# Kernel optimization log

Measured on AMD Instinct MI355X. Metric: run time of the kernel, lower is better.

## Reference

```python
import jax, jax.numpy as jnp
import numpy as np

N_NODES = 50000
N_EDGES = 1600000
IN_CH = 128
HID = 32
HEADS = 3
OUT_CH = 32
NEG_SLOPE = 0.2


def setup_inputs() -> dict:
    key = jax.random.key(0)
    ks = jax.random.split(key, 12)
    s = 0.05
    x = jax.random.normal(ks[0], (N_NODES, IN_CH), dtype=jnp.float32)
    edge_index = jax.random.randint(ks[1], (2, N_EDGES), 0, N_NODES, dtype=jnp.int64)
    W1 = jax.random.normal(ks[2], (IN_CH, HEADS * HID), dtype=jnp.float32) * s
    att_src1 = jax.random.normal(ks[3], (HEADS, HID), dtype=jnp.float32) * s
    att_dst1 = jax.random.normal(ks[4], (HEADS, HID), dtype=jnp.float32) * s
    b1 = jnp.zeros((HEADS * HID,), dtype=jnp.float32)
    W2 = jax.random.normal(ks[5], (HEADS * HID, OUT_CH), dtype=jnp.float32) * s
    att_src2 = jax.random.normal(ks[6], (1, OUT_CH), dtype=jnp.float32) * s
    att_dst2 = jax.random.normal(ks[7], (1, OUT_CH), dtype=jnp.float32) * s
    b2 = jnp.zeros((OUT_CH,), dtype=jnp.float32)
    Wp = jax.random.normal(ks[8], (OUT_CH, 1), dtype=jnp.float32) * s
    bp = jnp.zeros((1,), dtype=jnp.float32)
    return dict(x=x, edge_index=edge_index, W1=W1, att_src1=att_src1,
                att_dst1=att_dst1, b1=b1, W2=W2, att_src2=att_src2,
                att_dst2=att_dst2, b2=b2, Wp=Wp, bp=bp)


def gat_layer(x, src, dst, W, a_src, a_dst, b, heads, out_ch, concat):
    # PyG GATConv semantics: per-head linear, edge attention with leaky_relu,
    # softmax over incoming edges per destination node, scatter-add aggregate.
    N = x.shape[0]
    h = (x @ W).reshape(N, heads, out_ch)                 # [N,H,C]
    a_s = jnp.einsum('nhc,hc->nh', h, a_src)              # [N,H]
    a_d = jnp.einsum('nhc,hc->nh', h, a_dst)              # [N,H]
    e = jax.nn.leaky_relu(a_s[src] + a_d[dst], NEG_SLOPE) # [E,H]
    m = jax.ops.segment_max(e, dst, num_segments=N)       # stable softmax per dst
    p = jnp.exp(e - m[dst])
    s = jax.ops.segment_sum(p, dst, num_segments=N)
    alpha = p / (s[dst] + 1e-16)                          # [E,H]
    msg = h[src] * alpha[:, :, None]                      # [E,H,C]
    out = jax.ops.segment_sum(msg, dst, num_segments=N)   # [N,H,C]
    out = out.reshape(N, heads * out_ch) if concat else out.mean(axis=1)
    return out + b


def reference(x, edge_index, W1, att_src1, att_dst1, b1, W2, att_src2,
              att_dst2, b2, Wp, bp):
    N = x.shape[0]
    loop = jnp.arange(N, dtype=edge_index.dtype)
    src = jnp.concatenate([edge_index[0], loop])  # add self-loops (PyG default)
    dst = jnp.concatenate([edge_index[1], loop])
    h = gat_layer(x, src, dst, W1, att_src1, att_dst1, b1, HEADS, HID, True)
    h = jax.nn.elu(h)
    h = gat_layer(h, src, dst, W2, att_src2, att_dst2, b2, 1, OUT_CH, False)
    prob = jax.nn.sigmoid(h @ Wp + bp)                    # [N,1]
    return prob
```

## Files before the change

kernel.cpp:

```cpp
#include <hip/hip_runtime.h>
#include <hip/hip_bf16.h>
#include <math.h>


#define IN_CH 128
#define HID 32
#define HEADS 3
#define OUT_CH 32
#define NEG_SLOPE 0.2f

#define NBUCK_SHIFT 6
#define NBUCK_NODES 64
#define BCAP 2560
#define EPB 4096

typedef unsigned int uint;
typedef unsigned short ushort;
typedef short v8s __attribute__((ext_vector_type(8)));
typedef float v4f __attribute__((ext_vector_type(4)));
typedef uint v3u __attribute__((ext_vector_type(3)));

static __device__ __forceinline__ uint f2bf(float f) {
    uint u = __float_as_uint(f);
    return (u + 0x7FFFu + ((u >> 16) & 1u)) >> 16;
}
static __device__ __forceinline__ uint pk4fp8(float a, float b, float c, float d) {
    int r = 0;
    r = __builtin_amdgcn_cvt_pk_fp8_f32(a, b, r, false);
    r = __builtin_amdgcn_cvt_pk_fp8_f32(c, d, r, true);
    return (uint)r;
}
static __device__ __forceinline__ float elu_f(float o) {
    return o > 0.f ? o : __expf(o) - 1.f;
}
static __device__ __forceinline__ float frcp(float x) {
    return __builtin_amdgcn_rcpf(x);
}

#define LDA 136
#define LDC 100


__global__ __launch_bounds__(256) void k_pre(const float* __restrict__ W1,
                                             ushort* __restrict__ w1t,
                                             int* __restrict__ gcur) {
    int b = blockIdx.x, t = threadIdx.x;
    if (b < 12) {
        int base = b * 1024 + t * 4;
        #pragma unroll
        for (int j = 0; j < 4; ++j) {
            int idx = base + j;
            int n = idx >> 7, k = idx & 127;
            w1t[idx] = (ushort)f2bf(W1[k * 96 + n]);
        }
    } else {
        int i = (b - 12) * 256 + t;
        if (i < 1024) gcur[i] = 0;
    }
}


__global__ __launch_bounds__(256) void k_g1b(const float* __restrict__ x,
                                             const ushort* __restrict__ w1t,
                                             const float* __restrict__ as,
                                             const float* __restrict__ ad,
                                             uint* __restrict__ h1u,
                                             float* __restrict__ a_d1p,
                                             const int* __restrict__ ei,
                                             int E, int Etot, int B2, int G1,
                                             int* __restrict__ gcur,
                                             uint* __restrict__ stage, int N) {
    __shared__ __attribute__((aligned(16))) char raw[64 * LDC * 4];
    int tid = threadIdx.x;

    if ((int)blockIdx.x >= G1) {
        int* hist     = (int*)raw;
        int* runStart = hist + 1024;
        int* rankCtr  = runStart + 1024;
        for (int i = tid; i < 1024; i += 256) { hist[i] = 0; rankCtr[i] = 0; }
        __syncthreads();
        int base = ((int)blockIdx.x - G1) * EPB;

        uint rec[16];
        #pragma unroll
        for (int i = 0; i < 16; ++i) {
            int e = base + tid + i * 256;
            uint r = 0xFFFFFFFFu;
            if (e < Etot) {
                int s, d;
                if (e < E) { s = ei[e]; d = ei[E + e]; }
                else       { s = e - E; d = s; }
                r = ((uint)d << 16) | (uint)s;
                atomicAdd(&hist[d >> NBUCK_SHIFT], 1);
            }
            rec[i] = r;
        }
        __syncthreads();
        for (int i = tid; i < B2; i += 256) {
            int c = hist[i];
            if (c) runStart[i] = atomicAdd(&gcur[i], c);
        }
        __syncthreads();
        #pragma unroll
        for (int i = 0; i < 16; ++i) {
            uint r = rec[i];
            if (r != 0xFFFFFFFFu) {
                int b = (int)(r >> 16) >> NBUCK_SHIFT;
                int pos = runStart[b] + atomicAdd(&rankCtr[b], 1);
                if (pos < BCAP)
                    stage[(size_t)b * BCAP + pos] = r & 0x003FFFFFu;
            }
        }
        return;
    }

    ushort* sA  = (ushort*)raw;
    float*  sC  = (float*)raw;
    int b0 = blockIdx.x * 64;

    uint* sA32 = (uint*)sA;
    #pragma unroll
    for (int i = 0; i < 8; ++i) {
        int g = tid + i * 256;
        int row = g >> 5, c4 = g & 31;
        float4 v = make_float4(0.f, 0.f, 0.f, 0.f);
        int gn = b0 + row;
        if (gn < N) v = *(const float4*)(x + (size_t)gn * IN_CH + c4 * 4);
        sA32[row * 68 + c4 * 2]     = f2bf(v.x) | (f2bf(v.y) << 16);
        sA32[row * 68 + c4 * 2 + 1] = f2bf(v.z) | (f2bf(v.w) << 16);
    }
    __syncthreads();

    int l = tid & 63, w = tid >> 6;
    int m15 = l & 15, q = l >> 4;

    v8s afr[4];
    const ushort* arow = sA + (w * 16 + m15) * LDA + q * 8;
    #pragma unroll
    for (int kc = 0; kc < 4; ++kc) afr[kc] = *(const v8s*)(arow + kc * 32);

    v4f acc[6];
    #pragma unroll
    for (int cg = 0; cg < 6; ++cg) {
        acc[cg] = (v4f){0.f, 0.f, 0.f, 0.f};
        const ushort* browg = w1t + (cg * 16 + m15) * 128 + q * 8;
        #pragma unroll
        for (int kc = 0; kc < 4; ++kc) {
            v8s bfr = *(const v8s*)(browg + kc * 32);
            acc[cg] = __builtin_amdgcn_mfma_f32_16x16x32_bf16(afr[kc], bfr, acc[cg], 0, 0, 0);
        }
    }
    __syncthreads();
    #pragma unroll
    for (int cg = 0; cg < 6; ++cg) {
        int col = cg * 16 + m15;
        #pragma unroll
        for (int r = 0; r < 4; ++r)
            sC[(w * 16 + q * 4 + r) * LDC + col] = acc[cg][r];
    }
    __syncthreads();

    if (tid < 192) {
        int ln = tid / 3, h = tid - ln * 3;
        int node = b0 + ln;
        if (node < N) {
            const float* vs = as + h * 32;
            const float* vd = ad + h * 32;
            const float* row = sC + ln * LDC + h * 32;
            float4 s4 = make_float4(0.f, 0.f, 0.f, 0.f);
            float4 d4 = make_float4(0.f, 0.f, 0.f, 0.f);
            #pragma unroll
            for (int c = 0; c < 8; ++c) {
                float4 r = *(const float4*)(row + 4 * c);
                float4 a = *(const float4*)(vs + 4 * c);
                float4 bb = *(const float4*)(vd + 4 * c);
                s4.x += r.x * a.x;  s4.y += r.y * a.y;
                s4.z += r.z * a.z;  s4.w += r.w * a.w;
                d4.x += r.x * bb.x; d4.y += r.y * bb.y;
                d4.z += r.z * bb.z; d4.w += r.w * bb.w;
            }
            float s = (s4.x + s4.y) + (s4.z + s4.w);
            float d = (d4.x + d4.y) + (d4.z + d4.w);
            ((float*)h1u)[(size_t)node * 32 + 24 + h] = s;
            a_d1p[node * 4 + h] = d;
        }
    }
    {
        int node = tid >> 2, part = tid & 3;
        int gn = b0 + node;
        if (gn < N) {
            const float* row = sC + node * LDC;
            uint tmp[6];
            #pragma unroll
            for (int jj = 0; jj < 6; ++jj) {
                int j = part * 6 + jj;
                int dd = j / 3, slot = j - dd * 3;
                const float* p = row + slot * 32 + dd * 4;
                tmp[jj] = pk4fp8(p[0], p[1], p[2], p[3]);
            }
            uint* dst = h1u + (size_t)gn * 32 + part * 6;
            *(uint2*)(dst + 0) = make_uint2(tmp[0], tmp[1]);
            *(uint2*)(dst + 2) = make_uint2(tmp[2], tmp[3]);
            *(uint2*)(dst + 4) = make_uint2(tmp[4], tmp[5]);
        }
    }
}


__global__ __launch_bounds__(256) void k_sort(const uint* __restrict__ stage,
                                              const int* __restrict__ gcur,
                                              int* __restrict__ offs,
                                              ushort* __restrict__ edges,
                                              int N, int Etot, int B2) {
    __shared__ uint items[BCAP];
    __shared__ int red[256];
    __shared__ int lofs[NBUCK_NODES + 1];
    __shared__ int cursors[NBUCK_NODES];
    int t = threadIdx.x;
    int b = blockIdx.x;

    int partial = 0;
    for (int i = t; i < b; i += 256) partial += gcur[i];
    red[t] = partial;
    if (t < NBUCK_NODES) cursors[t] = 0;
    __syncthreads();
    #pragma unroll
    for (int s = 128; s > 0; s >>= 1) {
        if (t < s) red[t] += red[t + s];
        __syncthreads();
    }
    int gbase = red[0];
    int cnt = gcur[b]; if (cnt > BCAP) cnt = BCAP;

    for (int i = t; i < cnt; i += 256) items[i] = stage[(size_t)b * BCAP + i];
    __syncthreads();
    for (int i = t; i < cnt; i += 256) atomicAdd(&cursors[items[i] >> 16], 1);
    __syncthreads();
    if (t == 0) {
        int run = 0;
        for (int i = 0; i < NBUCK_NODES; ++i) { int v = cursors[i]; lofs[i] = run; run += v; }
        lofs[NBUCK_NODES] = run;
    }
    __syncthreads();
    int nodeBase = b << NBUCK_SHIFT;
    if (t < NBUCK_NODES && nodeBase + t < N) offs[nodeBase + t] = gbase + lofs[t];
    if (b == B2 - 1 && t == 0) offs[N] = Etot;
    if (t < NBUCK_NODES) cursors[t] = 0;
    __syncthreads();
    for (int i = t; i < cnt; i += 256) {
        uint it = items[i];
        int ln = (int)(it >> 16);
        int r = atomicAdd(&cursors[ln], 1);
        edges[gbase + lofs[ln] + r] = (ushort)(it & 0xFFFFu);
    }
}


#define W2LD 36

__global__ __launch_bounds__(256) void k_agg1g2(const int* __restrict__ offs,
                                                const ushort* __restrict__ edges,
                                                const uint* __restrict__ h1u,
                                                const float* __restrict__ a_d1p,
                                                const float* __restrict__ b1,
                                                const float* __restrict__ W2,
                                                const float* __restrict__ as2,
                                                const float* __restrict__ ad2,
                                                uint* __restrict__ h2u,
                                                float* __restrict__ a_d2, int N) {
    __shared__ __attribute__((aligned(16))) float sW2[96 * W2LD];
    __shared__ float ss2[32], sd2[32];
    __shared__ float rowbuf[8][96];

    int tid = threadIdx.x;
    #pragma unroll
    for (int i = 0; i < 3; ++i) {
        int gg = tid + i * 256;
        int k = gg >> 3, c4i = gg & 7;
        *(float4*)&sW2[k * W2LD + c4i * 4] = *(const float4*)(W2 + k * 32 + c4i * 4);
    }
    if (tid < 32) { ss2[tid] = as2[tid]; sd2[tid] = ad2[tid]; }
    __syncthreads();

    int w = tid >> 6;
    int lane = tid & 63;
    int half = lane >> 5, hl = lane & 31;
    int node = blockIdx.x * 8 + w * 2 + half;
    bool nvalid = node < N;
    int nodeC = nvalid ? node : (N - 1);
    int g = hl >> 3, d = hl & 7;
    const float4 adv = *(const float4*)(a_d1p + nodeC * 4);

    int off0 = offs[nodeC], off1 = offs[nodeC + 1];
    int deg = off1 - off0;
    if (deg < 0) deg = 0;
    int nIt = (deg + 3) >> 2;
    int nItO = __shfl_xor(nIt, 32);
    int itMax = nIt > nItO ? nIt : nItO;

    float a00 = 0.f, a01 = 0.f, a02 = 0.f, a03 = 0.f;
    float a10 = 0.f, a11 = 0.f, a12 = 0.f, a13 = 0.f;
    float a20 = 0.f, a21 = 0.f, a22 = 0.f, a23 = 0.f;
    float d0 = 0.f, d1 = 0.f, d2 = 0.f;

    #pragma unroll 2
    for (int i = 0; i < itMax; ++i) {
        int e = i * 4 + g;
        bool act = e < deg;
        int eidx = off0 + (act ? e : 0);
        uint src = (uint)edges[eidx];
        const uint* hr = h1u + src * 32u;
        float4 af = *(const float4*)(hr + 24);
        v3u wv = *(const v3u*)(hr + 3 * d);
        float z0 = af.x + adv.x, z1 = af.y + adv.y, z2 = af.z + adv.z;
        z0 = fmaxf(z0, NEG_SLOPE * z0);
        z1 = fmaxf(z1, NEG_SLOPE * z1);
        z2 = fmaxf(z2, NEG_SLOPE * z2);
        float p0 = __expf(z0), p1 = __expf(z1), p2 = __expf(z2);
        p0 = act ? p0 : 0.f;
        p1 = act ? p1 : 0.f;
        p2 = act ? p2 : 0.f;
        { auto lo = __builtin_amdgcn_cvt_pk_f32_fp8((int)wv[0], false);
          auto hi = __builtin_amdgcn_cvt_pk_f32_fp8((int)wv[0], true);
          a00 += p0 * lo[0]; a01 += p0 * lo[1];
          a02 += p0 * hi[0]; a03 += p0 * hi[1]; }
        { auto lo = __builtin_amdgcn_cvt_pk_f32_fp8((int)wv[1], false);
          auto hi = __builtin_amdgcn_cvt_pk_f32_fp8((int)wv[1], true);
          a10 += p1 * lo[0]; a11 += p1 * lo[1];
          a12 += p1 * hi[0]; a13 += p1 * hi[1]; }
        { auto lo = __builtin_amdgcn_cvt_pk_f32_fp8((int)wv[2], false);
          auto hi = __builtin_amdgcn_cvt_pk_f32_fp8((int)wv[2], true);
          a20 += p2 * lo[0]; a21 += p2 * lo[1];
          a22 += p2 * hi[0]; a23 += p2 * hi[1]; }
        d0 += p0; d1 += p1; d2 += p2;
    }

    #define REDF(v) { v += __shfl_xor(v, 8); v += __shfl_xor(v, 16); }
    REDF(a00) REDF(a01) REDF(a02) REDF(a03)
    REDF(a10) REDF(a11) REDF(a12) REDF(a13)
    REDF(a20) REDF(a21) REDF(a22) REDF(a23)
    REDF(d0) REDF(d1) REDF(d2)
    #undef REDF

    int rbrow = w * 2 + half;
    if (hl < 8) {
        float r0 = frcp(d0 + 1e-16f);
        float r1 = frcp(d1 + 1e-16f);
        float r2 = frcp(d2 + 1e-16f);
        float4 bv0 = *(const float4*)(b1 + 4 * hl);
        float4 bv1 = *(const float4*)(b1 + 32 + 4 * hl);
        float4 bv2 = *(const float4*)(b1 + 64 + 4 * hl);
        float4 v;
        v.x = elu_f(a00 * r0 + bv0.x);
        v.y = elu_f(a01 * r0 + bv0.y);
        v.z = elu_f(a02 * r0 + bv0.z);
        v.w = elu_f(a03 * r0 + bv0.w);
        *(float4*)&rowbuf[rbrow][4 * hl] = v;
        v.x = elu_f(a10 * r1 + bv1.x);
        v.y = elu_f(a11 * r1 + bv1.y);
        v.z = elu_f(a12 * r1 + bv1.z);
        v.w = elu_f(a13 * r1 + bv1.w);
        *(float4*)&rowbuf[rbrow][32 + 4 * hl] = v;
        v.x = elu_f(a20 * r2 + bv2.x);
        v.y = elu_f(a21 * r2 + bv2.y);
        v.z = elu_f(a22 * r2 + bv2.z);
        v.w = elu_f(a23 * r2 + bv2.w);
        *(float4*)&rowbuf[rbrow][64 + 4 * hl] = v;
    }

    int c4 = hl & 7, kg = hl >> 3;
    float4 accv = make_float4(0.f, 0.f, 0.f, 0.f);
    const float* rb = &rowbuf[rbrow][kg * 24];
    const float* wb = &sW2[kg * 24 * W2LD + c4 * 4];
    #pragma unroll 24
    for (int i = 0; i < 24; ++i) {
        float rv = rb[i];
        float4 wvv = *(const float4*)(wb + i * W2LD);
        accv.x += rv * wvv.x; accv.y += rv * wvv.y;
        accv.z += rv * wvv.z; accv.w += rv * wvv.w;
    }
    #define REDF(c) { c += __shfl_xor(c, 8); c += __shfl_xor(c, 16); }
    REDF(accv.x) REDF(accv.y) REDF(accv.z) REDF(accv.w)
    #undef REDF

    float4 sv = *(const float4*)&ss2[c4 * 4];
    float4 dv = *(const float4*)&sd2[c4 * 4];
    float ps = accv.x * sv.x + accv.y * sv.y + accv.z * sv.z + accv.w * sv.w;
    float pd = accv.x * dv.x + accv.y * dv.y + accv.z * dv.z + accv.w * dv.w;
    ps += __shfl_xor(ps, 1); ps += __shfl_xor(ps, 2); ps += __shfl_xor(ps, 4);
    pd += __shfl_xor(pd, 1); pd += __shfl_xor(pd, 2); pd += __shfl_xor(pd, 4);
    if (nvalid && hl < 8) {
        h2u[(size_t)node * 16 + c4] = pk4fp8(accv.x, accv.y, accv.z, accv.w);
        if (hl == 0) {
            ((float*)h2u)[(size_t)node * 16 + 8] = ps;
            a_d2[node] = pd;
        }
    }
}


__global__ __launch_bounds__(256) void k_agg2f(const int* __restrict__ offs,
                                               const ushort* __restrict__ edges,
                                               const uint* __restrict__ h2u,
                                               const float* __restrict__ a_d2,
                                               const float* __restrict__ b2,
                                               const float* __restrict__ Wp,
                                               const float* __restrict__ bp,
                                               float* __restrict__ out, int N) {
    int tid = threadIdx.x;
    int w = tid >> 6;
    int lane = tid & 63;
    int half = lane >> 5, hl = lane & 31;
    int node = blockIdx.x * 8 + w * 2 + half;
    bool nvalid = node < N;
    int nodeC = nvalid ? node : (N - 1);
    int g = hl >> 3, d = hl & 7;
    const float ad2u = a_d2[nodeC];

    int off0 = offs[nodeC], off1 = offs[nodeC + 1];
    int deg = off1 - off0;
    if (deg < 0) deg = 0;
    int nIt = (deg + 3) >> 2;
    int nItO = __shfl_xor(nIt, 32);
    int itMax = nIt > nItO ? nIt : nItO;

    float c0 = 0.f, c1 = 0.f, c2 = 0.f, c3 = 0.f, den = 0.f;

    #pragma unroll 2
    for (int i = 0; i < itMax; ++i) {
        int e = i * 4 + g;
        bool act = e < deg;
        int eidx = off0 + (act ? e : 0);
        uint src = (uint)edges[eidx];
        const uint* hr = h2u + src * 16u;
        float zf = *(const float*)(hr + 8);
        uint wvv = hr[d];
        float z = zf + ad2u;
        z = fmaxf(z, NEG_SLOPE * z);
        float p = __expf(z);
        p = act ? p : 0.f;
        auto lo = __builtin_amdgcn_cvt_pk_f32_fp8((int)wvv, false);
        auto hi = __builtin_amdgcn_cvt_pk_f32_fp8((int)wvv, true);
        c0 += p * lo[0]; c1 += p * lo[1];
        c2 += p * hi[0]; c3 += p * hi[1];
        den += p;
    }

    #define REDF(v) { v += __shfl_xor(v, 8); v += __shfl_xor(v, 16); }
    REDF(c0) REDF(c1) REDF(c2) REDF(c3) REDF(den)
    #undef REDF

    float4 bv = *(const float4*)(b2 + 4 * d);
    float4 wv = *(const float4*)(Wp + 4 * d);
    float r = frcp(den + 1e-16f);
    float v = (c0 * r + bv.x) * wv.x + (c1 * r + bv.y) * wv.y +
              (c2 * r + bv.z) * wv.z + (c3 * r + bv.w) * wv.w;
    v += __shfl_xor(v, 1);
    v += __shfl_xor(v, 2);
    v += __shfl_xor(v, 4);
    if (nvalid && hl == 0)
        out[node] = frcp(1.f + __expf(-(v + bp[0])));
}


extern "C" void kernel_launch(void* const* d_in, const int* in_sizes, int n_in,
                              void* d_out, int out_size, void* d_ws, size_t ws_size,
                              hipStream_t stream) {
    const float* x      = (const float*)d_in[0];
    const int*   ei     = (const int*)d_in[1];
    const float* W1     = (const float*)d_in[2];
    const float* att_s1 = (const float*)d_in[3];
    const float* att_d1 = (const float*)d_in[4];
    const float* b1     = (const float*)d_in[5];
    const float* W2     = (const float*)d_in[6];
    const float* att_s2 = (const float*)d_in[7];
    const float* att_d2 = (const float*)d_in[8];
    const float* b2     = (const float*)d_in[9];
    const float* Wp     = (const float*)d_in[10];
    const float* bp     = (const float*)d_in[11];
    float* out = (float*)d_out;

    const int N = in_sizes[0] / IN_CH;
    const int E = in_sizes[1] / 2;
    const int Etot = E + N;
    const int B2 = (N + NBUCK_NODES - 1) >> NBUCK_SHIFT;
    const int G1 = (N + 63) / 64;
    const int BK = (Etot + EPB - 1) / EPB;

    float*  ws    = (float*)d_ws;
    uint*   h1u   = (uint*)ws;
    float*  a_d1p = ws + (size_t)N * 32;
    int*    offs  = (int*)(a_d1p + (size_t)N * 4);
    ushort* edges = (ushort*)(offs + (N + 1));
    int*    gcur  = (int*)(edges + (((size_t)Etot + 1) & ~(size_t)1));
    uint*   stage = (uint*)(gcur + 1024);
    uint*   h2u   = stage + (size_t)B2 * BCAP;
    float*  a_d2  = (float*)(h2u + (size_t)N * 16);
    ushort* w1t   = (ushort*)(a_d2 + N);

    k_pre<<<16, 256, 0, stream>>>(W1, w1t, gcur);

    k_g1b<<<G1 + BK, 256, 0, stream>>>(x, w1t, att_s1, att_d1, h1u, a_d1p,
                                       ei, E, Etot, B2, G1, gcur, stage, N);
    k_sort<<<B2, 256, 0, stream>>>(stage, gcur, offs, edges, N, Etot, B2);

    k_agg1g2<<<(N + 7) / 8, 256, 0, stream>>>(offs, edges, h1u, a_d1p, b1, W2,
                                              att_s2, att_d2, h2u, a_d2, N);
    k_agg2f<<<(N + 7) / 8, 256, 0, stream>>>(offs, edges, h2u, a_d2,
                                             b2, Wp, bp, out, N);
}
```

Before: 201.2 us.

## Replace bucketed staging sort with per-node count, scan, and atomic scatter CSR build

Replaces the two-level bucket staging (write packed records into fixed-capacity buckets, then sort each bucket in shared memory) with a classic counting approach: per-node degree counts via global atomics, a per-bucket prefix scan that produces offsets and cursors, and a separate scatter kernel that re-reads edge_index and places sources with global atomics. This removes the staging buffer and its capacity limit but adds an extra kernel launch, a second read of edge_index, and 1.65M contended global atomics per pass. Edge order within each node becomes nondeterministic, so the floating-point summation order can vary from run to run.

```diff
diff --git a/kernel.cpp b/kernel.cpp
--- a/kernel.cpp
+++ b/kernel.cpp
@@ -11,7 +11,6 @@
 
 #define NBUCK_SHIFT 6
 #define NBUCK_NODES 64
-#define BCAP 2560
 #define EPB 4096
 
 typedef unsigned int uint;
@@ -43,7 +42,8 @@
 
 __global__ __launch_bounds__(256) void k_pre(const float* __restrict__ W1,
                                              ushort* __restrict__ w1t,
-                                             int* __restrict__ gcur) {
+                                             int* __restrict__ gcur,
+                                             int* __restrict__ cnt, int N) {
     int b = blockIdx.x, t = threadIdx.x;
     if (b < 12) {
         int base = b * 1024 + t * 4;
@@ -54,8 +54,13 @@
             w1t[idx] = (ushort)f2bf(W1[k * 96 + n]);
         }
     } else {
-        int i = (b - 12) * 256 + t;
-        if (i < 1024) gcur[i] = 0;
+        int base = (b - 12) * 1024 + t * 4;
+        #pragma unroll
+        for (int j = 0; j < 4; ++j) {
+            int id = base + j;
+            if (id < 1024) gcur[id] = 0;
+            else if (id - 1024 < N) cnt[id - 1024] = 0;
+        }
     }
 }
 
@@ -69,47 +74,28 @@
                                              const int* __restrict__ ei,
                                              int E, int Etot, int B2, int G1,
                                              int* __restrict__ gcur,
-                                             uint* __restrict__ stage, int N) {
+                                             int* __restrict__ cnt, int N) {
     __shared__ __attribute__((aligned(16))) char raw[64 * LDC * 4];
     int tid = threadIdx.x;
 
     if ((int)blockIdx.x >= G1) {
-        int* hist     = (int*)raw;
-        int* runStart = hist + 1024;
-        int* rankCtr  = runStart + 1024;
-        for (int i = tid; i < 1024; i += 256) { hist[i] = 0; rankCtr[i] = 0; }
+        int* hist = (int*)raw;
+        for (int i = tid; i < 1024; i += 256) hist[i] = 0;
         __syncthreads();
         int base = ((int)blockIdx.x - G1) * EPB;
-
-        uint rec[16];
         #pragma unroll
         for (int i = 0; i < 16; ++i) {
             int e = base + tid + i * 256;
-            uint r = 0xFFFFFFFFu;
             if (e < Etot) {
-                int s, d;
-                if (e < E) { s = ei[e]; d = ei[E + e]; }
-                else       { s = e - E; d = s; }
-                r = ((uint)d << 16) | (uint)s;
+                int d = (e < E) ? ei[E + e] : (e - E);
+                atomicAdd(&cnt[d], 1);
                 atomicAdd(&hist[d >> NBUCK_SHIFT], 1);
             }
-            rec[i] = r;
         }
         __syncthreads();
         for (int i = tid; i < B2; i += 256) {
             int c = hist[i];
-            if (c) runStart[i] = atomicAdd(&gcur[i], c);
-        }
-        __syncthreads();
-        #pragma unroll
-        for (int i = 0; i < 16; ++i) {
-            uint r = rec[i];
-            if (r != 0xFFFFFFFFu) {
-                int b = (int)(r >> 16) >> NBUCK_SHIFT;
-                int pos = runStart[b] + atomicAdd(&rankCtr[b], 1);
-                if (pos < BCAP)
-                    stage[(size_t)b * BCAP + pos] = r & 0x003FFFFFu;
-            }
+            if (c) atomicAdd(&gcur[i], c);
         }
         return;
     }
@@ -207,22 +193,18 @@
 }
 
 
-__global__ __launch_bounds__(256) void k_sort(const uint* __restrict__ stage,
-                                              const int* __restrict__ gcur,
+__global__ __launch_bounds__(256) void k_scan(const int* __restrict__ gcur,
+                                              const int* __restrict__ cnt,
                                               int* __restrict__ offs,
-                                              ushort* __restrict__ edges,
+                                              int* __restrict__ cur,
                                               int N, int Etot, int B2) {
-    __shared__ uint items[BCAP];
     __shared__ int red[256];
-    __shared__ int lofs[NBUCK_NODES + 1];
-    __shared__ int cursors[NBUCK_NODES];
-    int t = threadIdx.x;
-    int b = blockIdx.x;
+    __shared__ int snode[NBUCK_NODES + 1];
+    int t = threadIdx.x, b = blockIdx.x;
 
     int partial = 0;
     for (int i = t; i < b; i += 256) partial += gcur[i];
     red[t] = partial;
-    if (t < NBUCK_NODES) cursors[t] = 0;
     __syncthreads();
     #pragma unroll
     for (int s = 128; s > 0; s >>= 1) {
@@ -230,28 +212,39 @@
         __syncthreads();
     }
     int gbase = red[0];
-    int cnt = gcur[b]; if (cnt > BCAP) cnt = BCAP;
-
-    for (int i = t; i < cnt; i += 256) items[i] = stage[(size_t)b * BCAP + i];
-    __syncthreads();
-    for (int i = t; i < cnt; i += 256) atomicAdd(&cursors[items[i] >> 16], 1);
+    int nodeBase = b << NBUCK_SHIFT;
+    if (t < NBUCK_NODES)
+        snode[t] = (nodeBase + t < N) ? cnt[nodeBase + t] : 0;
     __syncthreads();
     if (t == 0) {
-        int run = 0;
-        for (int i = 0; i < NBUCK_NODES; ++i) { int v = cursors[i]; lofs[i] = run; run += v; }
-        lofs[NBUCK_NODES] = run;
-    }
-    __syncthreads();
-    int nodeBase = b << NBUCK_SHIFT;
-    if (t < NBUCK_NODES && nodeBase + t < N) offs[nodeBase + t] = gbase + lofs[t];
+        int run = gbase;
+        #pragma unroll
+        for (int i = 0; i < NBUCK_NODES; ++i) { int v = snode[i]; snode[i] = run; run += v; }
+    }
+    __syncthreads();
+    if (t < NBUCK_NODES && nodeBase + t < N) {
+        offs[nodeBase + t] = snode[t];
+        cur[nodeBase + t]  = snode[t];
+    }
     if (b == B2 - 1 && t == 0) offs[N] = Etot;
-    if (t < NBUCK_NODES) cursors[t] = 0;
-    __syncthreads();
-    for (int i = t; i < cnt; i += 256) {
-        uint it = items[i];
-        int ln = (int)(it >> 16);
-        int r = atomicAdd(&cursors[ln], 1);
-        edges[gbase + lofs[ln] + r] = (ushort)(it & 0xFFFFu);
+}
+
+
+__global__ __launch_bounds__(256) void k_scat(const int* __restrict__ ei,
+                                              int* __restrict__ cur,
+                                              ushort* __restrict__ edges,
+                                              int E, int Etot) {
+    int base = blockIdx.x * 1024 + threadIdx.x;
+    #pragma unroll
+    for (int j = 0; j < 4; ++j) {
+        int e = base + j * 256;
+        if (e < Etot) {
+            int s, d;
+            if (e < E) { s = ei[e]; d = ei[E + e]; }
+            else       { s = e - E; d = s; }
+            int pos = atomicAdd(&cur[d], 1);
+            edges[pos] = (ushort)s;
+        }
     }
 }
 
@@ -493,16 +486,19 @@
     int*    offs  = (int*)(a_d1p + (size_t)N * 4);
     ushort* edges = (ushort*)(offs + (N + 1));
     int*    gcur  = (int*)(edges + (((size_t)Etot + 1) & ~(size_t)1));
-    uint*   stage = (uint*)(gcur + 1024);
-    uint*   h2u   = stage + (size_t)B2 * BCAP;
+    int*    cnt   = gcur + 1024;
+    int*    cur   = cnt + N;
+    uint*   h2u   = (uint*)(cur + N);
     float*  a_d2  = (float*)(h2u + (size_t)N * 16);
     ushort* w1t   = (ushort*)(a_d2 + N);
 
-    k_pre<<<16, 256, 0, stream>>>(W1, w1t, gcur);
+    const int ZB = (1024 + N + 1023) / 1024;
+    k_pre<<<12 + ZB, 256, 0, stream>>>(W1, w1t, gcur, cnt, N);
 
     k_g1b<<<G1 + BK, 256, 0, stream>>>(x, w1t, att_s1, att_d1, h1u, a_d1p,
-                                       ei, E, Etot, B2, G1, gcur, stage, N);
-    k_sort<<<B2, 256, 0, stream>>>(stage, gcur, offs, edges, N, Etot, B2);
+                                       ei, E, Etot, B2, G1, gcur, cnt, N);
+    k_scan<<<B2, 256, 0, stream>>>(gcur, cnt, offs, cur, N, Etot, B2);
+    k_scat<<<(Etot + 1023) / 1024, 256, 0, stream>>>(ei, cur, edges, E, Etot);
 
     k_agg1g2<<<(N + 7) / 8, 256, 0, stream>>>(offs, edges, h1u, a_d1p, b1, W2,
                                               att_s2, att_d2, h2u, a_d2, N);
```

Result: slower. 343.9 us (+70.9%).
